# Performance work log

Hardware: AMD Instinct MI355X
Metric: run time of the kernel (lower is better)

The kernel has to match this reference:

```python
import jax, jax.numpy as jnp
import numpy as np

N_INPUT = 1024
BATCH = 65536


def setup_inputs() -> dict:
    key = jax.random.key(0)
    kx, kA, kB = jax.random.split(key, 3)
    # average half must be strictly positive for pow(average, alpha)
    x = jax.random.uniform(kx, (BATCH, 2 * N_INPUT), dtype=jnp.float32,
                           minval=0.1, maxval=2.0)
    A = jax.random.normal(kA, (N_INPUT,), dtype=jnp.float32)
    B = jax.random.normal(kB, (N_INPUT, N_INPUT), dtype=jnp.float32)
    C = jnp.zeros((1,), dtype=jnp.float32)
    alpha = jnp.ones((N_INPUT,), dtype=jnp.float32)
    return {"x": x, "A": A, "B": B, "C": C, "alpha": alpha}


def reference(x, A, B, C, alpha):
    n = A.shape[0]
    average = x[:, :n]          # [batch, n]
    numbers = x[:, -n:]         # [batch, n]
    organelle = numbers * jnp.power(average, alpha)  # [batch, n]
    linear = organelle @ A                                   # [batch]
    quad = jnp.einsum('bi,ij,bj->b', organelle, B, organelle)  # batched quadratic form
    return linear + quad + C    # C broadcasts [1] -> [batch]
```

## Files before the change

### kernel.cpp

```cpp
#include <hip/hip_runtime.h>
#include <hip/hip_bf16.h>

typedef __bf16 bf16x8 __attribute__((ext_vector_type(8)));
typedef __bf16 bf16x4 __attribute__((ext_vector_type(4)));
typedef float  f32x4  __attribute__((ext_vector_type(4)));

#define N_IN 1024
#define BM   64
#define NTHR 512

__global__ void convB_kernel(const float* __restrict__ B, __bf16* __restrict__ Bb) {
    int i = blockIdx.x * blockDim.x + threadIdx.x;
    f32x4 v = ((const f32x4*)B)[i];
    bf16x4 o;
    o[0] = (__bf16)v[0]; o[1] = (__bf16)v[1]; o[2] = (__bf16)v[2]; o[3] = (__bf16)v[3];
    ((bf16x4*)Bb)[i] = o;
}

template<bool USEBF>
__global__ __launch_bounds__(NTHR, 2)
void fused_kernel(const float* __restrict__ x, const float* __restrict__ A,
                  const float* __restrict__ Bf, const __bf16* __restrict__ Bb,
                  const float* __restrict__ Cp, const float* __restrict__ alpha,
                  float* __restrict__ out) {
    __shared__ __align__(16) __bf16 o_panel[BM * N_IN];
    __shared__ float rowsum[8][BM];

    const int t    = threadIdx.x;
    const int wave = t >> 6;
    const int lane = t & 63;
    const int lrow = lane & 15;
    const int lgrp = lane >> 4;
    const long blk_row = (long)blockIdx.x * BM;

    const int srow  = t >> 3;
    const int skoff = (t & 7) * 4;
    const float* xrow = x + (blk_row + srow) * (2 * N_IN);

    {
        int k = skoff;
        f32x4 sa  = *(const f32x4*)(xrow + k);
        f32x4 sn  = *(const f32x4*)(xrow + N_IN + k);
        f32x4 sal = *(const f32x4*)(alpha + k);
        bf16x4 w4;
        #pragma unroll
        for (int e = 0; e < 4; ++e) {
            float ov = sn[e] * __expf(sal[e] * __logf(sa[e]));
            w4[e] = (__bf16)ov;
        }
        int idx = srow * N_IN + ((k & ~7) ^ ((srow & 7) << 3)) + (k & 7);
        *(bf16x4*)&o_panel[idx] = w4;
    }
    __syncthreads();

    float rowpart[16];
    #pragma unroll
    for (int i = 0; i < 16; ++i) rowpart[i] = 0.f;

    #pragma unroll 1
    for (int pass = 0; pass < 2; ++pass) {
        const int colbase = pass * 512 + wave * 64;
        f32x4 acc[4][4];
        #pragma unroll
        for (int m = 0; m < 4; ++m)
            #pragma unroll
            for (int n = 0; n < 4; ++n)
                acc[m][n] = f32x4{0.f, 0.f, 0.f, 0.f};

        #pragma unroll 2
        for (int kc = 0; kc < 32; ++kc) {
            f32x4 sa, sn, sal;
            const bool staging = (pass == 0) && (kc + 1 < 32);
            if (staging) {
                int k = (kc + 1) * 32 + skoff;
                sa  = *(const f32x4*)(xrow + k);
                sn  = *(const f32x4*)(xrow + N_IN + k);
                sal = *(const f32x4*)(alpha + k);
            }
            bf16x8 afr[4];
            #pragma unroll
            for (int m = 0; m < 4; ++m) {
                int r  = m * 16 + lrow;
                int kk = kc * 32 + lgrp * 8;
                afr[m] = *(const bf16x8*)&o_panel[r * N_IN + (kk ^ ((r & 7) << 3))];
            }
            bf16x8 bfr[4];
            #pragma unroll
            for (int n = 0; n < 4; ++n) {
                int i  = colbase + n * 16 + lrow;
                int kk = kc * 32 + lgrp * 8;
                if constexpr (USEBF) {
                    bfr[n] = *(const bf16x8*)&Bb[(long)i * N_IN + kk];
                } else {
                    const float* p = Bf + (long)i * N_IN + kk;
                    f32x4 lo = *(const f32x4*)p;
                    f32x4 hi = *(const f32x4*)(p + 4);
                    #pragma unroll
                    for (int e = 0; e < 4; ++e) {
                        bfr[n][e]     = (__bf16)lo[e];
                        bfr[n][e + 4] = (__bf16)hi[e];
                    }
                }
            }
            #pragma unroll
            for (int m = 0; m < 4; ++m)
                #pragma unroll
                for (int n = 0; n < 4; ++n)
                    acc[m][n] = __builtin_amdgcn_mfma_f32_16x16x32_bf16(
                        afr[m], bfr[n], acc[m][n], 0, 0, 0);

            if (pass == 0) {
                if (staging) {
                    int k = (kc + 1) * 32 + skoff;
                    bf16x4 w4;
                    #pragma unroll
                    for (int e = 0; e < 4; ++e) {
                        float ov = sn[e] * __expf(sal[e] * __logf(sa[e]));
                        w4[e] = (__bf16)ov;
                    }
                    int idx = srow * N_IN + ((k & ~7) ^ ((srow & 7) << 3)) + (k & 7);
                    *(bf16x4*)&o_panel[idx] = w4;
                }
                __syncthreads();
            }
        }

        #pragma unroll
        for (int n = 0; n < 4; ++n) {
            int i = colbase + n * 16 + lrow;
            float Ai = A[i];
            #pragma unroll
            for (int m = 0; m < 4; ++m) {
                #pragma unroll
                for (int j = 0; j < 4; ++j) {
                    int r = m * 16 + lgrp * 4 + j;
                    float y  = acc[m][n][j] + Ai;
                    float ov = (float)o_panel[r * N_IN + ((i & ~7) ^ ((r & 7) << 3)) + (i & 7)];
                    rowpart[m * 4 + j] += y * ov;
                }
            }
        }
    }

    #pragma unroll
    for (int d = 1; d < 16; d <<= 1) {
        #pragma unroll
        for (int i = 0; i < 16; ++i)
            rowpart[i] += __shfl_xor(rowpart[i], d);
    }
    if (lrow == 0) {
        #pragma unroll
        for (int m = 0; m < 4; ++m)
            #pragma unroll
            for (int j = 0; j < 4; ++j)
                rowsum[wave][m * 16 + lgrp * 4 + j] = rowpart[m * 4 + j];
    }
    __syncthreads();
    if (t < BM) {
        float s = Cp[0];
        #pragma unroll
        for (int w = 0; w < 8; ++w) s += rowsum[w][t];
        out[blk_row + t] = s;
    }
}

extern "C" void kernel_launch(void* const* d_in, const int* in_sizes, int n_in,
                              void* d_out, int out_size, void* d_ws, size_t ws_size,
                              hipStream_t stream) {
    const float* x     = (const float*)d_in[0];
    const float* A     = (const float*)d_in[1];
    const float* B     = (const float*)d_in[2];
    const float* C     = (const float*)d_in[3];
    const float* alpha = (const float*)d_in[4];
    float* out = (float*)d_out;

    int batch = in_sizes[0] / (2 * N_IN);
    int grid  = batch / BM;

    bool useBf = (ws_size >= (size_t)(N_IN * N_IN * sizeof(__bf16)));
    if (useBf) {
        __bf16* Bb = (__bf16*)d_ws;
        int nvec = (N_IN * N_IN) / 4;
        convB_kernel<<<nvec / 256, 256, 0, stream>>>(B, Bb);
        fused_kernel<true><<<grid, NTHR, 0, stream>>>(x, A, nullptr, Bb, C, alpha, out);
    } else {
        fused_kernel<false><<<grid, NTHR, 0, stream>>>(x, A, B, nullptr, C, alpha, out);
    }
}
```

Before: 406.5 us.

## Merge two column passes into one with doubled accumulators and coarser sync

Replaces the two sequential 512-column passes with a single k-loop in which each wave accumulates both column halves at once (32 accumulator tiles). Each A-fragment read from LDS now feeds twice as many MFMAs. The organelle panel is prefetched 8 chunks ahead and the block synchronizes once per 8 k-chunks instead of every chunk. The cost is double the accumulator registers (128 VGPRs for acc alone), which risks spills or reduced occupancy under launch_bounds(512,2).

```diff
diff --git a/kernel.cpp b/kernel.cpp
--- a/kernel.cpp
+++ b/kernel.cpp
@@ -37,110 +37,107 @@
     const int skoff = (t & 7) * 4;
     const float* xrow = x + (blk_row + srow) * (2 * N_IN);
 
-    {
-        int k = skoff;
+    #pragma unroll
+    for (int c = 0; c < 8; ++c) {
+        int k = c * 32 + skoff;
         f32x4 sa  = *(const f32x4*)(xrow + k);
         f32x4 sn  = *(const f32x4*)(xrow + N_IN + k);
         f32x4 sal = *(const f32x4*)(alpha + k);
         bf16x4 w4;
         #pragma unroll
-        for (int e = 0; e < 4; ++e) {
-            float ov = sn[e] * __expf(sal[e] * __logf(sa[e]));
-            w4[e] = (__bf16)ov;
-        }
-        int idx = srow * N_IN + ((k & ~7) ^ ((srow & 7) << 3)) + (k & 7);
-        *(bf16x4*)&o_panel[idx] = w4;
+        for (int e = 0; e < 4; ++e)
+            w4[e] = (__bf16)(sn[e] * __expf(sal[e] * __logf(sa[e])));
+        *(bf16x4*)&o_panel[srow * N_IN + ((k & ~7) ^ ((srow & 7) << 3)) + (k & 7)] = w4;
     }
     __syncthreads();
+
+    f32x4 acc[2][4][4];
+    #pragma unroll
+    for (int h = 0; h < 2; ++h)
+        #pragma unroll
+        for (int m = 0; m < 4; ++m)
+            #pragma unroll
+            for (int n = 0; n < 4; ++n)
+                acc[h][m][n] = f32x4{0.f, 0.f, 0.f, 0.f};
+
+    #pragma unroll 1
+    for (int q = 0; q < 4; ++q) {
+        #pragma unroll
+        for (int kq = 0; kq < 8; ++kq) {
+            const int kc = q * 8 + kq;
+            const bool staging = (q < 3);
+            f32x4 sa, sn, sal;
+            if (staging) {
+                int k = (kc + 8) * 32 + skoff;
+                sa  = *(const f32x4*)(xrow + k);
+                sn  = *(const f32x4*)(xrow + N_IN + k);
+                sal = *(const f32x4*)(alpha + k);
+            }
+            const int kk = kc * 32 + lgrp * 8;
+            bf16x8 afr[4];
+            #pragma unroll
+            for (int m = 0; m < 4; ++m) {
+                int r = m * 16 + lrow;
+                afr[m] = *(const bf16x8*)&o_panel[r * N_IN + (kk ^ ((r & 7) << 3))];
+            }
+            bf16x8 bfr[2][4];
+            #pragma unroll
+            for (int h = 0; h < 2; ++h)
+                #pragma unroll
+                for (int n = 0; n < 4; ++n) {
+                    int i = h * 512 + wave * 64 + n * 16 + lrow;
+                    if constexpr (USEBF) {
+                        bfr[h][n] = *(const bf16x8*)&Bb[(long)i * N_IN + kk];
+                    } else {
+                        const float* p = Bf + (long)i * N_IN + kk;
+                        f32x4 lo = *(const f32x4*)p;
+                        f32x4 hi = *(const f32x4*)(p + 4);
+                        #pragma unroll
+                        for (int e = 0; e < 4; ++e) {
+                            bfr[h][n][e]     = (__bf16)lo[e];
+                            bfr[h][n][e + 4] = (__bf16)hi[e];
+                        }
+                    }
+                }
+            #pragma unroll
+            for (int h = 0; h < 2; ++h)
+                #pragma unroll
+                for (int m = 0; m < 4; ++m)
+                    #pragma unroll
+                    for (int n = 0; n < 4; ++n)
+                        acc[h][m][n] = __builtin_amdgcn_mfma_f32_16x16x32_bf16(
+                            afr[m], bfr[h][n], acc[h][m][n], 0, 0, 0);
+            if (staging) {
+                int k = (kc + 8) * 32 + skoff;
+                bf16x4 w4;
+                #pragma unroll
+                for (int e = 0; e < 4; ++e)
+                    w4[e] = (__bf16)(sn[e] * __expf(sal[e] * __logf(sa[e])));
+                *(bf16x4*)&o_panel[srow * N_IN + ((k & ~7) ^ ((srow & 7) << 3)) + (k & 7)] = w4;
+            }
+        }
+        __syncthreads();
+    }
 
     float rowpart[16];
     #pragma unroll
     for (int i = 0; i < 16; ++i) rowpart[i] = 0.f;
-
-    #pragma unroll 1
-    for (int pass = 0; pass < 2; ++pass) {
-        const int colbase = pass * 512 + wave * 64;
-        f32x4 acc[4][4];
+    #pragma unroll
+    for (int h = 0; h < 2; ++h)
         #pragma unroll
-        for (int m = 0; m < 4; ++m)
-            #pragma unroll
-            for (int n = 0; n < 4; ++n)
-                acc[m][n] = f32x4{0.f, 0.f, 0.f, 0.f};
-
-        #pragma unroll 2
-        for (int kc = 0; kc < 32; ++kc) {
-            f32x4 sa, sn, sal;
-            const bool staging = (pass == 0) && (kc + 1 < 32);
-            if (staging) {
-                int k = (kc + 1) * 32 + skoff;
-                sa  = *(const f32x4*)(xrow + k);
-                sn  = *(const f32x4*)(xrow + N_IN + k);
-                sal = *(const f32x4*)(alpha + k);
-            }
-            bf16x8 afr[4];
-            #pragma unroll
-            for (int m = 0; m < 4; ++m) {
-                int r  = m * 16 + lrow;
-                int kk = kc * 32 + lgrp * 8;
-                afr[m] = *(const bf16x8*)&o_panel[r * N_IN + (kk ^ ((r & 7) << 3))];
-            }
-            bf16x8 bfr[4];
-            #pragma unroll
-            for (int n = 0; n < 4; ++n) {
-                int i  = colbase + n * 16 + lrow;
-                int kk = kc * 32 + lgrp * 8;
-                if constexpr (USEBF) {
-                    bfr[n] = *(const bf16x8*)&Bb[(long)i * N_IN + kk];
-                } else {
-                    const float* p = Bf + (long)i * N_IN + kk;
-                    f32x4 lo = *(const f32x4*)p;
-                    f32x4 hi = *(const f32x4*)(p + 4);
-                    #pragma unroll
-                    for (int e = 0; e < 4; ++e) {
-                        bfr[n][e]     = (__bf16)lo[e];
-                        bfr[n][e + 4] = (__bf16)hi[e];
-                    }
-                }
-            }
+        for (int n = 0; n < 4; ++n) {
+            int i = h * 512 + wave * 64 + n * 16 + lrow;
+            float Ai = A[i];
             #pragma unroll
             for (int m = 0; m < 4; ++m)
                 #pragma unroll
-                for (int n = 0; n < 4; ++n)
-                    acc[m][n] = __builtin_amdgcn_mfma_f32_16x16x32_bf16(
-                        afr[m], bfr[n], acc[m][n], 0, 0, 0);
-
-            if (pass == 0) {
-                if (staging) {
-                    int k = (kc + 1) * 32 + skoff;
-                    bf16x4 w4;
-                    #pragma unroll
-                    for (int e = 0; e < 4; ++e) {
-                        float ov = sn[e] * __expf(sal[e] * __logf(sa[e]));
-                        w4[e] = (__bf16)ov;
-                    }
-                    int idx = srow * N_IN + ((k & ~7) ^ ((srow & 7) << 3)) + (k & 7);
-                    *(bf16x4*)&o_panel[idx] = w4;
-                }
-                __syncthreads();
-            }
-        }
-
-        #pragma unroll
-        for (int n = 0; n < 4; ++n) {
-            int i = colbase + n * 16 + lrow;
-            float Ai = A[i];
-            #pragma unroll
-            for (int m = 0; m < 4; ++m) {
-                #pragma unroll
                 for (int j = 0; j < 4; ++j) {
                     int r = m * 16 + lgrp * 4 + j;
-                    float y  = acc[m][n][j] + Ai;
+                    float y  = acc[h][m][n][j] + Ai;
                     float ov = (float)o_panel[r * N_IN + ((i & ~7) ^ ((r & 7) << 3)) + (i & 7)];
                     rowpart[m * 4 + j] += y * ov;
                 }
-            }
         }
-    }
 
     #pragma unroll
     for (int d = 1; d < 16; d <<= 1) {
```

After: 359.3 us. 1.13x faster.

## Warp-specialize producer waves and widen compute tile to single pass

Applied to the files above, without the earlier changes.

Adds two producer waves (640 threads) that load x, compute numbers*pow(average,alpha), and write the bf16 panel in chunks of 256 columns, while eight consumer waves run MFMAs on the previous chunk. Each consumer wave now covers 128 output columns with a 4x8 accumulator array, so the previous two-pass scheme and its per-k-step barrier go away and the block synchronizes only five times. This aims to overlap global loads and transcendental work with matrix math and to cut barrier overhead. It doubles accumulator registers per consumer wave, which with launch_bounds(640,2) risks spills or lower occupancy, and it makes the producer/consumer pipeline coarse-grained.

```diff
diff --git a/kernel.cpp b/kernel.cpp
--- a/kernel.cpp
+++ b/kernel.cpp
@@ -7,7 +7,7 @@
 
 #define N_IN 1024
 #define BM   64
-#define NTHR 512
+#define NTHR 640
 
 __global__ void convB_kernel(const float* __restrict__ B, __bf16* __restrict__ Bb) {
     int i = blockIdx.x * blockDim.x + threadIdx.x;
@@ -32,128 +32,116 @@
     const int lrow = lane & 15;
     const int lgrp = lane >> 4;
     const long blk_row = (long)blockIdx.x * BM;
+    const int  colbase = wave * 128;
 
-    const int srow  = t >> 3;
-    const int skoff = (t & 7) * 4;
-    const float* xrow = x + (blk_row + srow) * (2 * N_IN);
-
-    {
-        int k = skoff;
-        f32x4 sa  = *(const f32x4*)(xrow + k);
-        f32x4 sn  = *(const f32x4*)(xrow + N_IN + k);
-        f32x4 sal = *(const f32x4*)(alpha + k);
-        bf16x4 w4;
+    f32x4 acc[4][8];
+    #pragma unroll
+    for (int m = 0; m < 4; ++m)
         #pragma unroll
-        for (int e = 0; e < 4; ++e) {
-            float ov = sn[e] * __expf(sal[e] * __logf(sa[e]));
-            w4[e] = (__bf16)ov;
-        }
-        int idx = srow * N_IN + ((k & ~7) ^ ((srow & 7) << 3)) + (k & 7);
-        *(bf16x4*)&o_panel[idx] = w4;
-    }
-    __syncthreads();
-
-    float rowpart[16];
-    #pragma unroll
-    for (int i = 0; i < 16; ++i) rowpart[i] = 0.f;
+        for (int n = 0; n < 8; ++n)
+            acc[m][n] = f32x4{0.f, 0.f, 0.f, 0.f};
 
     #pragma unroll 1
-    for (int pass = 0; pass < 2; ++pass) {
-        const int colbase = pass * 512 + wave * 64;
-        f32x4 acc[4][4];
-        #pragma unroll
-        for (int m = 0; m < 4; ++m)
-            #pragma unroll
-            for (int n = 0; n < 4; ++n)
-                acc[m][n] = f32x4{0.f, 0.f, 0.f, 0.f};
-
-        #pragma unroll 2
-        for (int kc = 0; kc < 32; ++kc) {
-            f32x4 sa, sn, sal;
-            const bool staging = (pass == 0) && (kc + 1 < 32);
-            if (staging) {
-                int k = (kc + 1) * 32 + skoff;
-                sa  = *(const f32x4*)(xrow + k);
-                sn  = *(const f32x4*)(xrow + N_IN + k);
-                sal = *(const f32x4*)(alpha + k);
-            }
-            bf16x8 afr[4];
-            #pragma unroll
-            for (int m = 0; m < 4; ++m) {
-                int r  = m * 16 + lrow;
-                int kk = kc * 32 + lgrp * 8;
-                afr[m] = *(const bf16x8*)&o_panel[r * N_IN + (kk ^ ((r & 7) << 3))];
-            }
-            bf16x8 bfr[4];
-            #pragma unroll
-            for (int n = 0; n < 4; ++n) {
-                int i  = colbase + n * 16 + lrow;
-                int kk = kc * 32 + lgrp * 8;
-                if constexpr (USEBF) {
-                    bfr[n] = *(const bf16x8*)&Bb[(long)i * N_IN + kk];
-                } else {
-                    const float* p = Bf + (long)i * N_IN + kk;
-                    f32x4 lo = *(const f32x4*)p;
-                    f32x4 hi = *(const f32x4*)(p + 4);
+    for (int tick = 0; tick < 5; ++tick) {
+        if (wave < 8) {
+            if (tick >= 1) {
+                const int qq = tick - 1;
+                #pragma unroll
+                for (int kq = 0; kq < 8; ++kq) {
+                    const int kk = (qq * 8 + kq) * 32 + lgrp * 8;
+                    const int asw = kk ^ ((lrow & 7) << 3);
+                    bf16x8 afr[4];
                     #pragma unroll
-                    for (int e = 0; e < 4; ++e) {
-                        bfr[n][e]     = (__bf16)lo[e];
-                        bfr[n][e + 4] = (__bf16)hi[e];
+                    for (int m = 0; m < 4; ++m)
+                        afr[m] = *(const bf16x8*)&o_panel[(m * 16 + lrow) * N_IN + asw];
+                    bf16x8 bfr[8];
+                    #pragma unroll
+                    for (int n = 0; n < 8; ++n) {
+                        const int i = colbase + n * 16 + lrow;
+                        if constexpr (USEBF) {
+                            bfr[n] = *(const bf16x8*)&Bb[(long)i * N_IN + kk];
+                        } else {
+                            const float* p = Bf + (long)i * N_IN + kk;
+                            f32x4 lo = *(const f32x4*)p;
+                            f32x4 hi = *(const f32x4*)(p + 4);
+                            #pragma unroll
+                            for (int e = 0; e < 4; ++e) {
+                                bfr[n][e]     = (__bf16)lo[e];
+                                bfr[n][e + 4] = (__bf16)hi[e];
+                            }
+                        }
                     }
+                    #pragma unroll
+                    for (int m = 0; m < 4; ++m)
+                        #pragma unroll
+                        for (int n = 0; n < 8; ++n)
+                            acc[m][n] = __builtin_amdgcn_mfma_f32_16x16x32_bf16(
+                                afr[m], bfr[n], acc[m][n], 0, 0, 0);
                 }
             }
+        } else {
+            if (tick < 4) {
+                const int pt   = t - 512;
+                const int prow = pt >> 1;
+                const int pko  = (pt & 1) * 16;
+                const float* xr = x + (blk_row + prow) * (2 * N_IN);
+                const int sw = (prow & 7) << 3;
+                const int pbase = prow * N_IN;
+                #pragma unroll 2
+                for (int c = 0; c < 8; ++c) {
+                    const int kb = (tick * 8 + c) * 32 + pko;
+                    f32x4 va[4], vn[4], vl[4];
+                    #pragma unroll
+                    for (int u = 0; u < 4; ++u) {
+                        va[u] = *(const f32x4*)(xr + kb + 4 * u);
+                        vn[u] = *(const f32x4*)(xr + N_IN + kb + 4 * u);
+                        vl[u] = *(const f32x4*)(alpha + kb + 4 * u);
+                    }
+                    bf16x8 w[2];
+                    #pragma unroll
+                    for (int u = 0; u < 4; ++u)
+                        #pragma unroll
+                        for (int e = 0; e < 4; ++e) {
+                            float ov = vn[u][e] * __expf(vl[u][e] * __logf(va[u][e]));
+                            w[u >> 1][(u & 1) * 4 + e] = (__bf16)ov;
+                        }
+                    *(bf16x8*)&o_panel[pbase + (kb ^ sw)]       = w[0];
+                    *(bf16x8*)&o_panel[pbase + ((kb + 8) ^ sw)] = w[1];
+                }
+            }
+        }
+        __syncthreads();
+    }
+
+    if (wave < 8) {
+        float rp[16];
+        #pragma unroll
+        for (int i = 0; i < 16; ++i) rp[i] = 0.f;
+        #pragma unroll
+        for (int n = 0; n < 8; ++n) {
+            const int i = colbase + n * 16 + lrow;
+            const float Ai = A[i];
             #pragma unroll
             for (int m = 0; m < 4; ++m)
                 #pragma unroll
-                for (int n = 0; n < 4; ++n)
-                    acc[m][n] = __builtin_amdgcn_mfma_f32_16x16x32_bf16(
-                        afr[m], bfr[n], acc[m][n], 0, 0, 0);
-
-            if (pass == 0) {
-                if (staging) {
-                    int k = (kc + 1) * 32 + skoff;
-                    bf16x4 w4;
-                    #pragma unroll
-                    for (int e = 0; e < 4; ++e) {
-                        float ov = sn[e] * __expf(sal[e] * __logf(sa[e]));
-                        w4[e] = (__bf16)ov;
-                    }
-                    int idx = srow * N_IN + ((k & ~7) ^ ((srow & 7) << 3)) + (k & 7);
-                    *(bf16x4*)&o_panel[idx] = w4;
+                for (int j = 0; j < 4; ++j) {
+                    const int r = m * 16 + lgrp * 4 + j;
+                    float ov = (float)o_panel[r * N_IN + ((i & ~7) ^ ((r & 7) << 3)) + (i & 7)];
+                    rp[m * 4 + j] += (acc[m][n][j] + Ai) * ov;
                 }
-                __syncthreads();
-            }
         }
-
         #pragma unroll
-        for (int n = 0; n < 4; ++n) {
-            int i = colbase + n * 16 + lrow;
-            float Ai = A[i];
+        for (int d = 1; d < 16; d <<= 1)
             #pragma unroll
-            for (int m = 0; m < 4; ++m) {
+            for (int i = 0; i < 16; ++i)
+                rp[i] += __shfl_xor(rp[i], d);
+        if (lrow == 0) {
+            #pragma unroll
+            for (int m = 0; m < 4; ++m)
                 #pragma unroll
-                for (int j = 0; j < 4; ++j) {
-                    int r = m * 16 + lgrp * 4 + j;
-                    float y  = acc[m][n][j] + Ai;
-                    float ov = (float)o_panel[r * N_IN + ((i & ~7) ^ ((r & 7) << 3)) + (i & 7)];
-                    rowpart[m * 4 + j] += y * ov;
-                }
-            }
+                for (int j = 0; j < 4; ++j)
+                    rowsum[wave][m * 16 + lgrp * 4 + j] = rp[m * 4 + j];
         }
-    }
-
-    #pragma unroll
-    for (int d = 1; d < 16; d <<= 1) {
-        #pragma unroll
-        for (int i = 0; i < 16; ++i)
-            rowpart[i] += __shfl_xor(rowpart[i], d);
-    }
-    if (lrow == 0) {
-        #pragma unroll
-        for (int m = 0; m < 4; ++m)
-            #pragma unroll
-            for (int j = 0; j < 4; ++j)
-                rowsum[wave][m * 16 + lgrp * 4 + j] = rowpart[m * 4 + j];
     }
     __syncthreads();
     if (t < BM) {
```

After: 874.2 us. 2.15x slower.
